# Performance work log

Hardware: AMD Instinct MI355X
Metric: run time of the kernel (lower is better)

The kernel has to match this reference:

```python
import jax, jax.numpy as jnp
import numpy as np


def setup_inputs() -> dict:
    key = jax.random.key(0)
    k1, k2, k3, k4, k5 = jax.random.split(key, 5)
    B, S, E, H, D = 8, 1024, 1024, 8, 128  # batch, seq, embed, heads, hidden/head
    stdv = 1.0 / np.sqrt(D)
    return {
        "k": jax.random.normal(k1, (B, S, E), jnp.float32),
        "q": jax.random.normal(k2, (B, S, E), jnp.float32),
        "flag": 0,  # False: project q through w_qx
        "w_kx": jax.random.uniform(k3, (H, E, D), jnp.float32, -stdv, stdv),
        "w_qx": jax.random.uniform(k4, (H, E, D), jnp.float32, -stdv, stdv),
        "proj_w": jax.random.normal(k5, (E, H * D), jnp.float32) * 0.02,  # out_dim = embed_dim
        "proj_b": jnp.zeros((E,), jnp.float32),
    }


def reference(k, q, flag, w_kx, w_qx, proj_w, proj_b):
    H, E, D = w_kx.shape
    B, Sk, _ = k.shape
    Sq = q.shape[1]
    # per-head tanh projections: [H, B, S, D]
    kx = jnp.tanh(jnp.einsum("bse,hed->hbsd", k, w_kx))
    if flag:
        qx = jnp.broadcast_to(q[None], (H,) + q.shape)  # q already in hidden space
    else:
        qx = jnp.tanh(jnp.einsum("bse,hed->hbsd", q, w_qx))
    # scaled dot product scores [H, B, Sq, Sk]
    score = jnp.einsum("hbqd,hbkd->hbqk", qx, kx) / jnp.sqrt(jnp.float32(D))
    attn = jax.nn.softmax(score, axis=-1)
    out = jnp.einsum("hbqk,hbkd->hbqd", attn, kx)  # [H, B, Sq, D]
    # concat heads: [B, Sq, H*D], then output projection (dropout p=0 is identity)
    out = jnp.transpose(out, (1, 2, 0, 3)).reshape(B, Sq, H * D)
    return out @ proj_w.T + proj_b
```

## Files before the change

### kernel.cpp

```cpp
#include <hip/hip_runtime.h>

typedef unsigned short u16;
typedef unsigned int u32;
typedef __bf16 bf16x8 __attribute__((ext_vector_type(8)));
typedef float f32x4 __attribute__((ext_vector_type(4)));

#define MFMA16(a, b, c) __builtin_amdgcn_mfma_f32_16x16x32_bf16(a, b, c, 0, 0, 0)
#define EXP2(x) __builtin_amdgcn_exp2f(x)

typedef const void __attribute__((address_space(1)))* gas1_t;
typedef void __attribute__((address_space(3)))* las3_t;

__device__ __forceinline__ void gload16(const void* g, void* l) {
  __builtin_amdgcn_global_load_lds((gas1_t)g, (las3_t)l, 16, 0, 0);
}

__device__ __forceinline__ u16 f2bf(float f) {
  union { float f; u32 u; } v; v.f = f;
  u32 r = v.u + 0x7FFFu + ((v.u >> 16) & 1u);
  return (u16)(r >> 16);
}

__device__ __forceinline__ float fast_tanh(float x) {
  float xc = fminf(fmaxf(x, -20.f), 20.f);
  float t = EXP2(xc * 2.885390081777927f);
  return (t - 1.0f) * __builtin_amdgcn_rcpf(t + 1.0f);
}

__global__ __launch_bounds__(256) void cvt_kernel(const float* __restrict__ in,
                                                  u16* __restrict__ out, int n8) {
  int i = blockIdx.x * blockDim.x + threadIdx.x;
  int stride = gridDim.x * blockDim.x;
  for (; i < n8; i += stride) {
    const float4* p = (const float4*)(in + (size_t)i * 8);
    float4 a = p[0], b = p[1];
    u16 t[8];
    t[0] = f2bf(a.x); t[1] = f2bf(a.y); t[2] = f2bf(a.z); t[3] = f2bf(a.w);
    t[4] = f2bf(b.x); t[5] = f2bf(b.y); t[6] = f2bf(b.z); t[7] = f2bf(b.w);
    *(uint4*)(out + (size_t)i * 8) = *(uint4*)t;
  }
}

__global__ __launch_bounds__(256) void wtrans_kernel(const float* __restrict__ w,
                                                     u16* __restrict__ wT) {
  __shared__ float t[64][65];
  int h = blockIdx.z;
  int e0 = blockIdx.x * 64, d0 = blockIdx.y * 64;
  const float* src = w + (size_t)h * 1024 * 128;
  u16* dst = wT + (size_t)h * 128 * 1024;
  int tid = threadIdx.x;
  {
    int row = tid >> 2, c0 = (tid & 3) * 16;
#pragma unroll
    for (int i = 0; i < 4; ++i) {
      float4 v = *(const float4*)(src + (size_t)(e0 + row) * 128 + d0 + c0 + i * 4);
      t[row][c0 + i * 4 + 0] = v.x;
      t[row][c0 + i * 4 + 1] = v.y;
      t[row][c0 + i * 4 + 2] = v.z;
      t[row][c0 + i * 4 + 3] = v.w;
    }
  }
  __syncthreads();
  {
    int dl = tid >> 2, c0 = (tid & 3) * 16;
    u16 tmp[16];
#pragma unroll
    for (int i = 0; i < 16; ++i) tmp[i] = f2bf(t[c0 + i][dl]);
    u16* o = dst + (size_t)(d0 + dl) * 1024 + e0 + c0;
    *(uint4*)o = *(uint4*)tmp;
    *(uint4*)(o + 8) = *(uint4*)(tmp + 8);
  }
}


template <int NI>
__device__ __forceinline__ void stageT(u16* dst, const u16* src, int K, int koff,
                                       int wid, int lane) {
#pragma unroll
  for (int i = 0; i < NI; ++i) {
    int c = (wid * NI + i) * 64 + lane;
    int lr = c >> 3, dsl = c & 7;
    int ssl = dsl ^ (lr & 7);
    int grow = lr * 2 + (ssl >> 2);
    int gk = koff + (ssl & 3) * 8;
    gload16((const char*)src + ((size_t)grow * K + gk) * 2, (char*)dst + c * 16);
  }
}

__device__ __forceinline__ bf16x8 ldfrag(const u16* half, int rp, int g) {
  int lr = rp >> 1;
  int slot = (((rp & 1) << 2) | g) ^ (lr & 7);
  return *(const bf16x8*)(half + lr * 64 + slot * 8);
}

template <int BM>
__device__ __forceinline__ void gemm8_core(const u16* __restrict__ Ab,
                                           const u16* __restrict__ Bb,
                                           int K, u16* lds,
                                           f32x4 (&acc)[BM / 32][4]) {
  constexpr int MF = BM / 32, MH = MF / 2;
  constexpr int AH = (BM / 2) * 64;
  constexpr int BH = 128 * 64;
  constexpr int BUF = 2 * AH + 2 * BH;
  constexpr int NIA = BM / 128;
  const int tid = threadIdx.x, lane = tid & 63, wid = tid >> 6;
  const int wr = wid >> 2, wc = wid & 3, l15 = lane & 15, g = lane >> 4;
  const int nkt = K >> 6;
  const int arow0 = wr * (BM / 2);

#define VWAITN()                                                                \
  do {                                                                          \
    if constexpr (NIA == 2) asm volatile("s_waitcnt vmcnt(4)" ::: "memory");    \
    else                    asm volatile("s_waitcnt vmcnt(3)" ::: "memory");    \
  } while (0)

  stageT<NIA>(lds, Ab, K, 0, wid, lane);
  stageT<2>(lds + 2 * AH, Bb, K, 0, wid, lane);
  stageT<NIA>(lds + AH, Ab, K, 32, wid, lane);
  stageT<2>(lds + 2 * AH + BH, Bb, K, 32, wid, lane);

  for (int t = 0; t < nkt; ++t) {
    const int cur = t & 1;
    u16* Ac = lds + cur * BUF;
    u16* Bc = Ac + 2 * AH;
    u16* An = lds + (cur ^ 1) * BUF;
    u16* Bn = An + 2 * AH;
    const bool pf = (t + 1 < nkt);
    const int k1 = (t + 1) * 64;
    bf16x8 af[MH], bb[4];

    VWAITN();
    __builtin_amdgcn_s_barrier();
    if (pf) stageT<NIA>(An, Ab, K, k1, wid, lane);
#pragma unroll
    for (int m = 0; m < MH; ++m) af[m] = ldfrag(Ac, arow0 + m * 16 + l15, g);
#pragma unroll
    for (int n = 0; n < 4; ++n) bb[n] = ldfrag(Bc, wc * 64 + n * 16 + l15, g);
    __builtin_amdgcn_s_setprio(1);
#pragma unroll
    for (int m = 0; m < MH; ++m)
#pragma unroll
      for (int n = 0; n < 4; ++n) acc[m][n] = MFMA16(af[m], bb[n], acc[m][n]);
    __builtin_amdgcn_s_setprio(0);

    __builtin_amdgcn_s_barrier();
    if (pf) stageT<2>(Bn, Bb, K, k1, wid, lane);
#pragma unroll
    for (int m = 0; m < MH; ++m)
      af[m] = ldfrag(Ac, arow0 + (MH + m) * 16 + l15, g);
    __builtin_amdgcn_s_setprio(1);
#pragma unroll
    for (int m = 0; m < MH; ++m)
#pragma unroll
      for (int n = 0; n < 4; ++n)
        acc[MH + m][n] = MFMA16(af[m], bb[n], acc[MH + m][n]);
    __builtin_amdgcn_s_setprio(0);

    if (pf) VWAITN();
    else asm volatile("s_waitcnt vmcnt(0)" ::: "memory");
    __builtin_amdgcn_s_barrier();
    if (pf) stageT<NIA>(An + AH, Ab, K, k1 + 32, wid, lane);
#pragma unroll
    for (int m = 0; m < MH; ++m) af[m] = ldfrag(Ac + AH, arow0 + m * 16 + l15, g);
#pragma unroll
    for (int n = 0; n < 4; ++n) bb[n] = ldfrag(Bc + BH, wc * 64 + n * 16 + l15, g);
    __builtin_amdgcn_s_setprio(1);
#pragma unroll
    for (int m = 0; m < MH; ++m)
#pragma unroll
      for (int n = 0; n < 4; ++n) acc[m][n] = MFMA16(af[m], bb[n], acc[m][n]);
    __builtin_amdgcn_s_setprio(0);

    __builtin_amdgcn_s_barrier();
    if (pf) stageT<2>(Bn + BH, Bb, K, k1 + 32, wid, lane);
#pragma unroll
    for (int m = 0; m < MH; ++m)
      af[m] = ldfrag(Ac + AH, arow0 + (MH + m) * 16 + l15, g);
    __builtin_amdgcn_s_setprio(1);
#pragma unroll
    for (int m = 0; m < MH; ++m)
#pragma unroll
      for (int n = 0; n < 4; ++n)
        acc[MH + m][n] = MFMA16(af[m], bb[n], acc[MH + m][n]);
    __builtin_amdgcn_s_setprio(0);
    __builtin_amdgcn_s_barrier();
  }
#undef VWAITN
}

__global__ __launch_bounds__(512, 2) void gemm_tanh_kernel(
    const u16* __restrict__ Ak, const u16* __restrict__ Aq,
    const u16* __restrict__ wTk, const u16* __restrict__ wTq,
    u16* __restrict__ kxo, u16* __restrict__ qxo) {
  __shared__ alignas(16) u16 lds[2 * (2 * 128 * 64 + 2 * 128 * 64)];
  const u16* A; const u16* W; u16* C;
  if (blockIdx.z == 0) { A = Ak; W = wTk; C = kxo; }
  else { A = Aq; W = wTq; C = qxo; }
  int mBase = blockIdx.x * 256;
  int nBase = blockIdx.y * 256;
  f32x4 acc[8][4];
#pragma unroll
  for (int i = 0; i < 8; ++i)
#pragma unroll
    for (int j = 0; j < 4; ++j) acc[i][j] = (f32x4){0.f, 0.f, 0.f, 0.f};
  gemm8_core<256>(A + (size_t)mBase * 1024, W + (size_t)nBase * 1024, 1024,
                  lds, acc);
  const int lane = threadIdx.x & 63, wid = threadIdx.x >> 6;
  const int wr = wid >> 2, wc = wid & 3, l15 = lane & 15, g = lane >> 4;
#pragma unroll
  for (int mf = 0; mf < 8; ++mf)
#pragma unroll
    for (int nf = 0; nf < 4; ++nf)
#pragma unroll
      for (int j = 0; j < 4; ++j) {
        int m = mBase + wr * 128 + mf * 16 + g * 4 + j;
        int n = nBase + wc * 64 + nf * 16 + l15;
        int h = n >> 7, d = n & 127;
        C[(size_t)h * 8192 * 128 + (size_t)m * 128 + d] =
            f2bf(fast_tanh(acc[mf][nf][j]));
      }
}

__global__ __launch_bounds__(256) void transpose_kernel(const u16* __restrict__ kx,
                                                        u16* __restrict__ kxT) {
  __shared__ u16 t[64][72];
  int hb = blockIdx.z;
  const u16* src = kx + (size_t)hb * 1024 * 128;
  u16* dst = kxT + (size_t)hb * 128 * 1024;
  int s0 = blockIdx.x * 64, d0 = blockIdx.y * 64;
  int tid = threadIdx.x;
#pragma unroll
  for (int r = 0; r < 2; ++r) {
    int row = r * 32 + (tid >> 3), c8 = (tid & 7) * 8;
    uint4 v = *(const uint4*)(src + (size_t)(s0 + row) * 128 + d0 + c8);
    *(uint4*)&t[row][c8] = v;
  }
  __syncthreads();
#pragma unroll
  for (int r = 0; r < 2; ++r) {
    int dl = r * 32 + (tid >> 3), s8 = (tid & 7) * 8;
    u16 tmp[8];
#pragma unroll
    for (int i = 0; i < 8; ++i) tmp[i] = t[s8 + i][dl];
    *(uint4*)(dst + (size_t)(d0 + dl) * 1024 + s0 + s8) = *(uint4*)tmp;
  }
}

__global__ __launch_bounds__(256, 2) void attn_kernel(const u16* __restrict__ qx,
                                                      const u16* __restrict__ kx,
                                                      const u16* __restrict__ kxT,
                                                      u16* __restrict__ X) {
  __shared__ alignas(16) u16 Klds[2][64 * 128];
  __shared__ alignas(16) u16 Vlds[2][128 * 64];
  __shared__ alignas(16) u16 Plds[4][32 * 64];
  const int tid = threadIdx.x, lane = tid & 63, wid = tid >> 6;
  const int g = lane >> 4;
  const int hb = blockIdx.x, qt = blockIdx.y, h = hb >> 3, b = hb & 7;
  const u16* qxh = qx + ((size_t)h * 8192 + (size_t)b * 1024) * 128;
  const u16* kxh = kx + ((size_t)h * 8192 + (size_t)b * 1024) * 128;
  const u16* kxTh = kxT + (size_t)hb * 128 * 1024;
  const int q0 = qt * 128 + wid * 32;
  const float SC = 0.08838834764831845f * 1.44269504088896340f;

#define STAGE(buf, kt_)                                                        \
  do {                                                                         \
    _Pragma("unroll") for (int i_ = 0; i_ < 4; ++i_) {                         \
      int cIdx = (wid * 4 + i_) * 64 + lane;                                   \
      {                                                                        \
        int row = cIdx >> 4, slot = cIdx & 15;                                 \
        int src = slot ^ (row & 7);                                            \
        gload16((const char*)kxh + (size_t)((kt_) * 64 + row) * 256 + src * 16,\
                (char*)&Klds[buf][0] + (wid * 4 + i_) * 1024);                 \
      }                                                                        \
      {                                                                        \
        int row = cIdx >> 3, slot = cIdx & 7;                                  \
        int src = slot ^ (row & 7);                                            \
        gload16((const char*)kxTh + (size_t)row * 2048 + (kt_) * 128 + src * 16,\
                (char*)&Vlds[buf][0] + (wid * 4 + i_) * 1024);                 \
      }                                                                        \
    }                                                                          \
  } while (0)

  bf16x8 qa[2][4];
#pragma unroll
  for (int m = 0; m < 2; ++m)
#pragma unroll
    for (int kc = 0; kc < 4; ++kc)
      qa[m][kc] = *(const bf16x8*)(qxh + (size_t)(q0 + m * 16 + (lane & 15)) * 128
                                   + kc * 32 + g * 8);

  f32x4 os[2][8];
#pragma unroll
  for (int i = 0; i < 2; ++i)
#pragma unroll
    for (int j = 0; j < 8; ++j) os[i][j] = (f32x4){0.f, 0.f, 0.f, 0.f};
  float lsum[2] = {0.f, 0.f};

  u16* Pw = &Plds[wid][0];

  STAGE(0, 0);

  for (int kt = 0; kt < 16; ++kt) {
    const int cur = kt & 1;
    if (kt < 15) {
      STAGE(cur ^ 1, kt + 1);
      asm volatile("s_waitcnt vmcnt(8)" ::: "memory");
    } else {
      asm volatile("s_waitcnt vmcnt(0)" ::: "memory");
    }
    __builtin_amdgcn_s_barrier();

    const u16* Kc = &Klds[cur][0];
    const u16* Vc = &Vlds[cur][0];

    f32x4 sa[4][2];
#pragma unroll
    for (int i = 0; i < 4; ++i)
#pragma unroll
      for (int j = 0; j < 2; ++j) sa[i][j] = (f32x4){0.f, 0.f, 0.f, 0.f};
    __builtin_amdgcn_s_setprio(1);
#pragma unroll
    for (int kc = 0; kc < 4; ++kc) {
      bf16x8 kb[4];
#pragma unroll
      for (int t = 0; t < 4; ++t) {
        int row = t * 16 + (lane & 15);
        int ch = kc * 4 + g;
        kb[t] = *(const bf16x8*)(Kc + row * 128 + ((ch ^ (row & 7)) << 3));
      }
#pragma unroll
      for (int t = 0; t < 4; ++t)
#pragma unroll
        for (int m = 0; m < 2; ++m)
          sa[t][m] = MFMA16(kb[t], qa[m][kc], sa[t][m]);
    }
    __builtin_amdgcn_s_setprio(0);

#pragma unroll
    for (int m = 0; m < 2; ++m) {
      int q = m * 16 + (lane & 15);
      int rowb = q * 128, q7 = q & 7;
#pragma unroll
      for (int t = 0; t < 4; ++t) {
        float p0 = EXP2(sa[t][m][0] * SC);
        float p1 = EXP2(sa[t][m][1] * SC);
        float p2 = EXP2(sa[t][m][2] * SC);
        float p3 = EXP2(sa[t][m][3] * SC);
        lsum[m] += (p0 + p1) + (p2 + p3);
        uint2 pk;
        pk.x = (u32)f2bf(p0) | ((u32)f2bf(p1) << 16);
        pk.y = (u32)f2bf(p2) | ((u32)f2bf(p3) << 16);
        int slot = (2 * t + (g >> 1)) ^ q7;
        *(uint2*)((char*)Pw + rowb + slot * 16 + 8 * (g & 1)) = pk;
      }
    }

    __builtin_amdgcn_s_setprio(1);
#pragma unroll
    for (int kc2 = 0; kc2 < 2; ++kc2) {
      bf16x8 pa[2], vb[8];
#pragma unroll
      for (int m = 0; m < 2; ++m) {
        int q = m * 16 + (lane & 15);
        int slot = (g + 4 * kc2) ^ (q & 7);
        pa[m] = *(const bf16x8*)((char*)Pw + q * 128 + slot * 16);
      }
#pragma unroll
      for (int nd = 0; nd < 8; ++nd) {
        int row = nd * 16 + (lane & 15);
        int ch = kc2 * 4 + g;
        vb[nd] = *(const bf16x8*)(Vc + row * 64 + ((ch ^ (row & 7)) << 3));
      }
#pragma unroll
      for (int m = 0; m < 2; ++m)
#pragma unroll
        for (int nd = 0; nd < 8; ++nd)
          os[m][nd] = MFMA16(pa[m], vb[nd], os[m][nd]);
    }
    __builtin_amdgcn_s_setprio(0);
    __builtin_amdgcn_s_barrier();
  }
#undef STAGE

#pragma unroll
  for (int m = 0; m < 2; ++m) {
    float s = lsum[m];
    s += __shfl_xor(s, 16);
    s += __shfl_xor(s, 32);
    lsum[m] = s;
  }

#pragma unroll
  for (int m = 0; m < 2; ++m)
#pragma unroll
    for (int j = 0; j < 4; ++j) {
      float tot = __shfl(lsum[m], 4 * g + j, 64);
      float inv = 1.f / tot;
      int qrow = b * 1024 + q0 + m * 16 + g * 4 + j;
#pragma unroll
      for (int nd = 0; nd < 8; ++nd) {
        int col = h * 128 + nd * 16 + (lane & 15);
        X[(size_t)qrow * 1024 + col] = f2bf(os[m][nd][j] * inv);
      }
    }
}

__global__ __launch_bounds__(512, 2) void gemm_bias_kernel(
    const u16* __restrict__ X, const u16* __restrict__ pw,
    const float* __restrict__ pb, float* __restrict__ out) {
  __shared__ alignas(16) u16 lds[2 * (2 * 64 * 64 + 2 * 128 * 64)];
  int mBase = blockIdx.x * 128;
  int nBase = blockIdx.y * 256;
  f32x4 acc[4][4];
#pragma unroll
  for (int i = 0; i < 4; ++i)
#pragma unroll
    for (int j = 0; j < 4; ++j) acc[i][j] = (f32x4){0.f, 0.f, 0.f, 0.f};
  gemm8_core<128>(X + (size_t)mBase * 1024, pw + (size_t)nBase * 1024, 1024,
                  lds, acc);
  const int lane = threadIdx.x & 63, wid = threadIdx.x >> 6;
  const int wr = wid >> 2, wc = wid & 3, l15 = lane & 15, g = lane >> 4;
#pragma unroll
  for (int nf = 0; nf < 4; ++nf) {
    int e = nBase + wc * 64 + nf * 16 + l15;
    float bv = pb[e];
#pragma unroll
    for (int mf = 0; mf < 4; ++mf)
#pragma unroll
      for (int j = 0; j < 4; ++j) {
        int m = mBase + wr * 64 + mf * 16 + g * 4 + j;
        out[(size_t)m * 1024 + e] = acc[mf][nf][j] + bv;
      }
  }
}

extern "C" void kernel_launch(void* const* d_in, const int* in_sizes, int n_in,
                              void* d_out, int out_size, void* d_ws, size_t ws_size,
                              hipStream_t stream) {
  const float* k = (const float*)d_in[0];
  const float* q = (const float*)d_in[1];
  const float* wk = (const float*)d_in[3];
  const float* wq = (const float*)d_in[4];
  const float* pw = (const float*)d_in[5];
  const float* pb = (const float*)d_in[6];
  float* out = (float*)d_out;
  char* ws = (char*)d_ws;

  u16* kbf = (u16*)(ws);
  u16* qbf = (u16*)(ws + (16ull << 20));
  u16* wTk = (u16*)(ws + (32ull << 20));
  u16* wTq = (u16*)(ws + (34ull << 20));
  u16* pwb = (u16*)(ws + (36ull << 20));
  u16* kx  = (u16*)(ws + (38ull << 20));
  u16* qx  = (u16*)(ws + (54ull << 20));
  u16* kxT = (u16*)(ws + (70ull << 20));
  u16* X   = kbf;

  cvt_kernel<<<2048, 256, 0, stream>>>(k, kbf, 1048576);
  cvt_kernel<<<2048, 256, 0, stream>>>(q, qbf, 1048576);
  cvt_kernel<<<512, 256, 0, stream>>>(pw, pwb, 131072);
  wtrans_kernel<<<dim3(16, 2, 8), 256, 0, stream>>>(wk, wTk);
  wtrans_kernel<<<dim3(16, 2, 8), 256, 0, stream>>>(wq, wTq);
  gemm_tanh_kernel<<<dim3(32, 4, 2), 512, 0, stream>>>(kbf, qbf, wTk, wTq, kx, qx);
  transpose_kernel<<<dim3(16, 2, 64), 256, 0, stream>>>(kx, kxT);
  attn_kernel<<<dim3(64, 8), 256, 0, stream>>>(qx, kx, kxT, X);
  gemm_bias_kernel<<<dim3(64, 4), 512, 0, stream>>>(X, pwb, pb, out);
}
```

Measured before the change: 138.2 us.

## Restructure GEMM core into quadrant-based 8-wave ping-pong with full-K tiles

Reworks the bf16 GEMM main loop so each LDS half-buffer holds half the M (or N) rows across the full 64-wide K slice, instead of splitting by K. Each iteration now runs four MFMA quadrants (A-half x B-half), interleaving fragment loads, prefetch of the next tile's half-buffers and barriers around each quadrant. The aim is finer-grained overlap of global-to-LDS loads with MFMA work and fewer fragment reloads per K step. It adds more barriers per iteration and hand-tuned vmcnt waits whose correctness depends on the exact load counts.

```diff
diff --git a/kernel.cpp b/kernel.cpp
--- a/kernel.cpp
+++ b/kernel.cpp
@@ -73,119 +73,126 @@
 }
 
 
-template <int NI>
-__device__ __forceinline__ void stageT(u16* dst, const u16* src, int K, int koff,
-                                       int wid, int lane) {
-#pragma unroll
-  for (int i = 0; i < NI; ++i) {
-    int c = (wid * NI + i) * 64 + lane;
-    int lr = c >> 3, dsl = c & 7;
-    int ssl = dsl ^ (lr & 7);
-    int grow = lr * 2 + (ssl >> 2);
-    int gk = koff + (ssl & 3) * 8;
-    gload16((const char*)src + ((size_t)grow * K + gk) * 2, (char*)dst + c * 16);
-  }
-}
-
-__device__ __forceinline__ bf16x8 ldfrag(const u16* half, int rp, int g) {
-  int lr = rp >> 1;
-  int slot = (((rp & 1) << 2) | g) ^ (lr & 7);
-  return *(const bf16x8*)(half + lr * 64 + slot * 8);
-}
-
 template <int BM>
 __device__ __forceinline__ void gemm8_core(const u16* __restrict__ Ab,
                                            const u16* __restrict__ Bb,
                                            int K, u16* lds,
                                            f32x4 (&acc)[BM / 32][4]) {
-  constexpr int MF = BM / 32, MH = MF / 2;
+  constexpr int MH = BM / 64;
+  constexpr int HR = BM / 4;
   constexpr int AH = (BM / 2) * 64;
   constexpr int BH = 128 * 64;
   constexpr int BUF = 2 * AH + 2 * BH;
-  constexpr int NIA = BM / 128;
+  constexpr int LA = BM / 128;
   const int tid = threadIdx.x, lane = tid & 63, wid = tid >> 6;
   const int wr = wid >> 2, wc = wid & 3, l15 = lane & 15, g = lane >> 4;
   const int nkt = K >> 6;
-  const int arow0 = wr * (BM / 2);
-
-#define VWAITN()                                                                \
-  do {                                                                          \
-    if constexpr (NIA == 2) asm volatile("s_waitcnt vmcnt(4)" ::: "memory");    \
-    else                    asm volatile("s_waitcnt vmcnt(3)" ::: "memory");    \
-  } while (0)
-
-  stageT<NIA>(lds, Ab, K, 0, wid, lane);
-  stageT<2>(lds + 2 * AH, Bb, K, 0, wid, lane);
-  stageT<NIA>(lds + AH, Ab, K, 32, wid, lane);
-  stageT<2>(lds + 2 * AH + BH, Bb, K, 32, wid, lane);
-
+  const int arow = wr * HR;
+  const int brow = wc * 32;
+
+  auto stageA = [&](u16* dstHalf, int mh, int kt) {
+#pragma unroll
+    for (int i = 0; i < LA; ++i) {
+      int c = (wid * LA + i) * 64 + lane;
+      int rr = c >> 3, src = (c & 7) ^ (rr & 7);
+      int grow = (rr / HR) * (2 * HR) + mh * HR + (rr % HR);
+      gload16((const char*)Ab + ((size_t)grow * K + kt * 64 + src * 8) * 2,
+              (char*)dstHalf + c * 16);
+    }
+  };
+  auto stageB = [&](u16* dstHalf, int nh, int kt) {
+#pragma unroll
+    for (int i = 0; i < 2; ++i) {
+      int c = (wid * 2 + i) * 64 + lane;
+      int cc = c >> 3, src = (c & 7) ^ (cc & 7);
+      int gcol = (cc >> 5) * 64 + nh * 32 + (cc & 31);
+      gload16((const char*)Bb + ((size_t)gcol * K + kt * 64 + src * 8) * 2,
+              (char*)dstHalf + c * 16);
+    }
+  };
+
+#define LDAF(half)                                                              \
+  _Pragma("unroll") for (int m = 0; m < MH; ++m)                                \
+  _Pragma("unroll") for (int kc = 0; kc < 2; ++kc) {                            \
+    int r_ = arow + m * 16 + l15;                                               \
+    af[m][kc] = *(const bf16x8*)((half) + r_ * 64 + (((kc * 4 + g) ^ (r_ & 7)) << 3)); \
+  }
+#define LDBF(half)                                                              \
+  _Pragma("unroll") for (int n = 0; n < 2; ++n)                                 \
+  _Pragma("unroll") for (int kc = 0; kc < 2; ++kc) {                            \
+    int r_ = brow + n * 16 + l15;                                               \
+    bb[n][kc] = *(const bf16x8*)((half) + r_ * 64 + (((kc * 4 + g) ^ (r_ & 7)) << 3)); \
+  }
+#define MFMAQ(MB, NB)                                                           \
+  __builtin_amdgcn_s_setprio(1);                                                \
+  _Pragma("unroll") for (int m = 0; m < MH; ++m)                                \
+  _Pragma("unroll") for (int n = 0; n < 2; ++n)                                 \
+  _Pragma("unroll") for (int kc = 0; kc < 2; ++kc)                              \
+    acc[(MB) * MH + m][(NB) * 2 + n] =                                          \
+        MFMA16(af[m][kc], bb[n][kc], acc[(MB) * MH + m][(NB) * 2 + n]);         \
+  __builtin_amdgcn_s_setprio(0);
+
+  stageA(lds, 0, 0);
+  stageB(lds + 2 * AH, 0, 0);
+  stageA(lds + AH, 1, 0);
+  stageB(lds + 2 * AH + BH, 1, 0);
+  if constexpr (BM == 256) asm volatile("s_waitcnt vmcnt(4)" ::: "memory");
+  else                     asm volatile("s_waitcnt vmcnt(3)" ::: "memory");
+  __builtin_amdgcn_s_barrier();
+
+  bf16x8 af[MH][2], bb[2][2];
   for (int t = 0; t < nkt; ++t) {
     const int cur = t & 1;
-    u16* Ac = lds + cur * BUF;
-    u16* Bc = Ac + 2 * AH;
-    u16* An = lds + (cur ^ 1) * BUF;
-    u16* Bn = An + 2 * AH;
+    u16* A0c = lds + cur * BUF;
+    u16* A1c = A0c + AH;
+    u16* B0c = A0c + 2 * AH;
+    u16* B1c = B0c + BH;
+    u16* A0n = lds + (cur ^ 1) * BUF;
+    u16* A1n = A0n + AH;
+    u16* B0n = A0n + 2 * AH;
+    u16* B1n = B0n + BH;
     const bool pf = (t + 1 < nkt);
-    const int k1 = (t + 1) * 64;
-    bf16x8 af[MH], bb[4];
-
-    VWAITN();
-    __builtin_amdgcn_s_barrier();
-    if (pf) stageT<NIA>(An, Ab, K, k1, wid, lane);
-#pragma unroll
-    for (int m = 0; m < MH; ++m) af[m] = ldfrag(Ac, arow0 + m * 16 + l15, g);
-#pragma unroll
-    for (int n = 0; n < 4; ++n) bb[n] = ldfrag(Bc, wc * 64 + n * 16 + l15, g);
-    __builtin_amdgcn_s_setprio(1);
-#pragma unroll
-    for (int m = 0; m < MH; ++m)
-#pragma unroll
-      for (int n = 0; n < 4; ++n) acc[m][n] = MFMA16(af[m], bb[n], acc[m][n]);
-    __builtin_amdgcn_s_setprio(0);
-
-    __builtin_amdgcn_s_barrier();
-    if (pf) stageT<2>(Bn, Bb, K, k1, wid, lane);
-#pragma unroll
-    for (int m = 0; m < MH; ++m)
-      af[m] = ldfrag(Ac, arow0 + (MH + m) * 16 + l15, g);
-    __builtin_amdgcn_s_setprio(1);
-#pragma unroll
-    for (int m = 0; m < MH; ++m)
-#pragma unroll
-      for (int n = 0; n < 4; ++n)
-        acc[MH + m][n] = MFMA16(af[m], bb[n], acc[MH + m][n]);
-    __builtin_amdgcn_s_setprio(0);
-
-    if (pf) VWAITN();
-    else asm volatile("s_waitcnt vmcnt(0)" ::: "memory");
-    __builtin_amdgcn_s_barrier();
-    if (pf) stageT<NIA>(An + AH, Ab, K, k1 + 32, wid, lane);
-#pragma unroll
-    for (int m = 0; m < MH; ++m) af[m] = ldfrag(Ac + AH, arow0 + m * 16 + l15, g);
-#pragma unroll
-    for (int n = 0; n < 4; ++n) bb[n] = ldfrag(Bc + BH, wc * 64 + n * 16 + l15, g);
-    __builtin_amdgcn_s_setprio(1);
-#pragma unroll
-    for (int m = 0; m < MH; ++m)
-#pragma unroll
-      for (int n = 0; n < 4; ++n) acc[m][n] = MFMA16(af[m], bb[n], acc[m][n]);
-    __builtin_amdgcn_s_setprio(0);
-
-    __builtin_amdgcn_s_barrier();
-    if (pf) stageT<2>(Bn + BH, Bb, K, k1 + 32, wid, lane);
-#pragma unroll
-    for (int m = 0; m < MH; ++m)
-      af[m] = ldfrag(Ac + AH, arow0 + (MH + m) * 16 + l15, g);
-    __builtin_amdgcn_s_setprio(1);
-#pragma unroll
-    for (int m = 0; m < MH; ++m)
-#pragma unroll
-      for (int n = 0; n < 4; ++n)
-        acc[MH + m][n] = MFMA16(af[m], bb[n], acc[MH + m][n]);
-    __builtin_amdgcn_s_setprio(0);
-    __builtin_amdgcn_s_barrier();
-  }
-#undef VWAITN
+    const int k1 = t + 1;
+
+    asm volatile("s_waitcnt vmcnt(2)" ::: "memory");
+    LDAF(A0c);
+    LDBF(B0c);
+    if (pf) stageA(A0n, 0, k1);
+    __builtin_amdgcn_s_barrier();
+    MFMAQ(0, 0);
+    __builtin_amdgcn_s_barrier();
+
+    if (pf) {
+      if constexpr (BM == 256) asm volatile("s_waitcnt vmcnt(2)" ::: "memory");
+      else                     asm volatile("s_waitcnt vmcnt(1)" ::: "memory");
+    } else {
+      asm volatile("s_waitcnt vmcnt(0)" ::: "memory");
+    }
+    LDAF(A1c);
+    if (pf) stageB(B0n, 0, k1);
+    __builtin_amdgcn_s_barrier();
+    MFMAQ(1, 0);
+    __builtin_amdgcn_s_barrier();
+
+    LDBF(B1c);
+    if (pf) stageA(A1n, 1, k1);
+    __builtin_amdgcn_s_barrier();
+    MFMAQ(1, 1);
+    __builtin_amdgcn_s_barrier();
+
+    if (pf) {
+      if constexpr (BM == 256) asm volatile("s_waitcnt vmcnt(2)" ::: "memory");
+      else                     asm volatile("s_waitcnt vmcnt(1)" ::: "memory");
+    }
+    LDAF(A0c);
+    if (pf) stageB(B1n, 1, k1);
+    __builtin_amdgcn_s_barrier();
+    MFMAQ(0, 1);
+    __builtin_amdgcn_s_barrier();
+  }
+#undef LDAF
+#undef LDBF
+#undef MFMAQ
 }
 
 __global__ __launch_bounds__(512, 2) void gemm_tanh_kernel(
```

Result: no change. 137.5 us (-0.5%).
